# Optimization experiments

Hardware: AMD Instinct MI355X
Metric: run time of the kernel (lower is better)

Reference implementation:

```python
import jax, jax.numpy as jnp
import numpy as np

B, H, W, C, HEADS, SR = 4, 64, 64, 256, 8, 2
D = C // HEADS            # head dim = 32
SCALE = D ** -0.5
EPS = 1e-6


def _conv(x, w, stride, pad, groups):
    return jax.lax.conv_general_dilated(
        x, w, (stride, stride), [(pad, pad), (pad, pad)],
        feature_group_count=groups,
        dimension_numbers=('NCHW', 'OIHW', 'NCHW'))


def setup_inputs() -> dict:
    key = jax.random.key(0)
    ks = jax.random.split(key, 9)
    s = lambda fan: 1.0 / np.sqrt(fan)
    return {
        'x': jax.random.normal(ks[0], (B, H * W, C), jnp.float32),
        'dw_w': jax.random.normal(ks[1], (C, 1, 3, 3), jnp.float32) * s(9),
        'dw_b': jnp.zeros((C,), jnp.float32),
        'pw_w': jax.random.normal(ks[2], (C, C, 1, 1), jnp.float32) * s(C),
        'pw_b': jnp.zeros((C,), jnp.float32),
        'sr_w': jax.random.normal(ks[3], (C, 1, 3, 3), jnp.float32) * s(9),
        'ln_g': jnp.ones((C,), jnp.float32),
        'ln_b': jnp.zeros((C,), jnp.float32),
        'kv_w': jax.random.normal(ks[4], (2 * C, C), jnp.float32) * s(C),
        'kv_b': jnp.zeros((2 * C,), jnp.float32),
        'proj_w': jax.random.normal(ks[5], (C, C), jnp.float32) * s(C),
        'proj_b': jnp.zeros((C,), jnp.float32),
    }


def reference(x, dw_w, dw_b, pw_w, pw_b, sr_w, ln_g, ln_b, kv_w, kv_b, proj_w, proj_b):
    Bx, N, Cx = x.shape
    # Q path: depthwise-separable conv on the spatial layout
    xq = x.reshape(Bx, H, W, Cx).transpose(0, 3, 1, 2)          # (B,C,H,W)
    q = _conv(xq, dw_w, 1, 1, Cx) + dw_b[None, :, None, None]    # depthwise 3x3
    q = _conv(q, pw_w, 1, 0, 1) + pw_b[None, :, None, None]      # pointwise 1x1
    # 'b (h d) l w -> b h (l w) d'
    q = q.reshape(Bx, HEADS, D, H * W).transpose(0, 1, 3, 2)     # (B,h,N,d)

    # SR path for K/V: strided depthwise conv + LayerNorm
    x_ = _conv(xq, sr_w, SR, SR // 2, Cx)                        # (B,C,H/SR,W/SR)
    x_ = x_.reshape(Bx, Cx, -1).transpose(0, 2, 1)               # (B,M,C)
    mu = jnp.mean(x_, axis=-1, keepdims=True)
    var = jnp.mean(jnp.square(x_ - mu), axis=-1, keepdims=True)
    x_ = (x_ - mu) * jax.lax.rsqrt(var + EPS) * ln_g + ln_b

    kv = x_ @ kv_w.T + kv_b                                      # (B,M,2C)
    M = kv.shape[1]
    kv = kv.reshape(Bx, M, 2, HEADS, D).transpose(2, 0, 3, 1, 4) # (2,B,h,M,d)
    k, v = kv[0], kv[1]

    attn = jnp.einsum('bhnd,bhmd->bhnm', q, k) * SCALE           # (B,h,N,M)
    attn = jax.nn.softmax(attn, axis=-1)
    out = jnp.einsum('bhnm,bhmd->bhnd', attn, v)                 # (B,h,N,d)
    out = out.transpose(0, 2, 1, 3).reshape(Bx, N, Cx)           # (B,N,C)
    return out @ proj_w.T + proj_b
```

## Files before the change

kernel.cpp:

```cpp
#include <hip/hip_runtime.h>
#include <math.h>

#define BB 4
#define HH 64
#define WW 64
#define CC 256
#define NN 4096
#define MM 1024
#define LN_EPS 1e-6f
#define SLF (0.17677669529663687f * 1.4426950408889634f)

typedef __attribute__((ext_vector_type(8)))  short short8;
typedef __attribute__((ext_vector_type(16))) float f32x16;

__device__ __forceinline__ ushort f2bf(float f) {
  unsigned u = __builtin_bit_cast(unsigned, f);
  u += 0x7fffu + ((u >> 16) & 1u);
  return (ushort)(u >> 16);
}
__device__ __forceinline__ float bf2f(ushort h) {
  unsigned u = ((unsigned)h) << 16;
  return __builtin_bit_cast(float, u);
}
#if __has_builtin(__builtin_amdgcn_exp2f)
#define EXP2F(x) __builtin_amdgcn_exp2f(x)
#else
#define EXP2F(x) exp2f(x)
#endif

__global__ __launch_bounds__(256) void dwconv_kernel(
    const float* __restrict__ x, const float* __restrict__ w,
    const float* __restrict__ bias, ushort* __restrict__ out) {
  int c = threadIdx.x;
  int y = blockIdx.x >> 1, hf = blockIdx.x & 1;
  int b = blockIdx.y;
  float wr[9];
#pragma unroll
  for (int i = 0; i < 9; ++i) wr[i] = w[c * 9 + i];
  float bi = bias[c];
  const float* xb = x + (size_t)b * NN * CC + c;
  int x0 = hf * 32;
  bool okT = (y > 0), okB = (y < 63);
  float a0, a1, a2, b0, b1, b2;
  if (x0 == 0) {
    a0 = a1 = a2 = 0.f;
  } else {
    a0 = okT ? xb[(size_t)((y - 1) * 64 + x0 - 1) * CC] : 0.f;
    a1 = xb[(size_t)(y * 64 + x0 - 1) * CC];
    a2 = okB ? xb[(size_t)((y + 1) * 64 + x0 - 1) * CC] : 0.f;
  }
  b0 = okT ? xb[(size_t)((y - 1) * 64 + x0) * CC] : 0.f;
  b1 = xb[(size_t)(y * 64 + x0) * CC];
  b2 = okB ? xb[(size_t)((y + 1) * 64 + x0) * CC] : 0.f;
  ushort* ob = out + ((size_t)b * NN + y * 64) * CC + c;
#pragma unroll 8
  for (int xx = x0; xx < x0 + 32; ++xx) {
    float c0v, c1v, c2v;
    if (xx < 63) {
      c0v = okT ? xb[(size_t)((y - 1) * 64 + xx + 1) * CC] : 0.f;
      c1v = xb[(size_t)(y * 64 + xx + 1) * CC];
      c2v = okB ? xb[(size_t)((y + 1) * 64 + xx + 1) * CC] : 0.f;
    } else {
      c0v = c1v = c2v = 0.f;
    }
    float acc = bi;
    acc += a0 * wr[0] + b0 * wr[1] + c0v * wr[2];
    acc += a1 * wr[3] + b1 * wr[4] + c1v * wr[5];
    acc += a2 * wr[6] + b2 * wr[7] + c2v * wr[8];
    ob[(size_t)xx * CC] = f2bf(acc);
    a0 = b0; a1 = b1; a2 = b2;
    b0 = c0v; b1 = c1v; b2 = c2v;
  }
}

__global__ __launch_bounds__(256) void srln_kernel(
    const float* __restrict__ x, const float* __restrict__ w,
    const float* __restrict__ g, const float* __restrict__ beta,
    ushort* __restrict__ out) {
  int c = threadIdx.x;
  int m = blockIdx.x;
  int b = blockIdx.y;
  int my = m >> 5, mx = m & 31;
  const float* xb = x + (size_t)b * NN * CC + c;
  float acc = 0.f;
#pragma unroll
  for (int dy = 0; dy < 3; ++dy) {
    int iy = 2 * my + dy - 1;
    if (iy < 0 || iy >= HH) continue;
#pragma unroll
    for (int dx = 0; dx < 3; ++dx) {
      int ix = 2 * mx + dx - 1;
      if (ix < 0 || ix >= WW) continue;
      acc += xb[(size_t)(iy * WW + ix) * CC] * w[c * 9 + dy * 3 + dx];
    }
  }
  float v1 = acc, v2 = acc * acc;
#pragma unroll
  for (int s = 1; s < 64; s <<= 1) {
    v1 += __shfl_xor(v1, s);
    v2 += __shfl_xor(v2, s);
  }
  __shared__ float r1[4], r2[4];
  int lane = c & 63, wv = c >> 6;
  if (lane == 0) { r1[wv] = v1; r2[wv] = v2; }
  __syncthreads();
  float s1 = r1[0] + r1[1] + r1[2] + r1[3];
  float s2 = r2[0] + r2[1] + r2[2] + r2[3];
  float mu = s1 * (1.f / 256.f);
  float var = s2 * (1.f / 256.f) - mu * mu;
  float yv = (acc - mu) * rsqrtf(var + LN_EPS) * g[c] + beta[c];
  out[((size_t)b * MM + m) * CC + c] = f2bf(yv);
}

template <int MODE>
__global__ __launch_bounds__(256) void gemm_mfma(
    const ushort* __restrict__ A, const ushort* __restrict__ A2,
    const float* __restrict__ W, const float* __restrict__ bias,
    void* __restrict__ out0, void* __restrict__ out1) {
  extern __shared__ ushort smem[];
  constexpr int AS = 128 * 40, WS = 64 * 40;
  constexpr int OA = 0, OW = AS, OA2 = AS + WS, OW2 = 2 * AS + WS;
  constexpr int BUF = (MODE == 2) ? 2 * (AS + WS) : (AS + WS);
  ushort* bf0 = smem;
  ushort* bf1 = smem + BUF;

  int t = threadIdx.x;
  int lane = t & 63, w = t >> 6;
  int l31 = lane & 31, half = lane >> 5;
  int r0 = blockIdx.x * 128;
  int c0 = blockIdx.y * 64;
  const bool vmode = (MODE == 1) && (c0 >= 256);

  int rowA = t >> 2, kq = (t & 3) * 8;

  f32x16 acc[2];
#pragma unroll
  for (int ct = 0; ct < 2; ++ct)
#pragma unroll
    for (int i = 0; i < 16; ++i) acc[ct][i] = 0.f;

  short8 ra0, ra1, ra20, ra21;
  float4 rw0, rw1;

  auto prefetch = [&](int kc) {
    ra0 = *(const short8*)&A[(size_t)(r0 + rowA) * 256 + kc + kq];
    ra1 = *(const short8*)&A[(size_t)(r0 + rowA + 64) * 256 + kc + kq];
    const float* wp = &W[(size_t)(c0 + rowA) * 256 + kc + kq];
    rw0 = *(const float4*)wp;
    rw1 = *(const float4*)(wp + 4);
    if constexpr (MODE == 2) {
      ra20 = *(const short8*)&A2[(size_t)(r0 + rowA) * 256 + kc + kq];
      ra21 = *(const short8*)&A2[(size_t)(r0 + rowA + 64) * 256 + kc + kq];
    }
  };

  auto store = [&](ushort* buf) {
    *(short8*)&buf[OA + rowA * 40 + kq] = ra0;
    *(short8*)&buf[OA + (rowA + 64) * 40 + kq] = ra1;
    float vals[8] = {rw0.x, rw0.y, rw0.z, rw0.w, rw1.x, rw1.y, rw1.z, rw1.w};
    short8 hi;
#pragma unroll
    for (int j = 0; j < 8; ++j) hi[j] = (short)f2bf(vals[j]);
    *(short8*)&buf[OW + rowA * 40 + kq] = hi;
    if constexpr (MODE == 2) {
      *(short8*)&buf[OA2 + rowA * 40 + kq] = ra20;
      *(short8*)&buf[OA2 + (rowA + 64) * 40 + kq] = ra21;
      short8 lo;
#pragma unroll
      for (int j = 0; j < 8; ++j)
        lo[j] = (short)f2bf(vals[j] - bf2f((ushort)hi[j]));
      *(short8*)&buf[OW2 + rowA * 40 + kq] = lo;
    }
  };

  auto compute = [&](const ushort* buf) {
#pragma unroll
    for (int ks = 0; ks < 2; ++ks) {
      int ro = (w * 32 + l31) * 40 + ks * 16 + half * 8;
      short8 af = *(const short8*)&buf[OA + ro];
      short8 af2;
      if constexpr (MODE == 2) af2 = *(const short8*)&buf[OA2 + ro];
#pragma unroll
      for (int ct = 0; ct < 2; ++ct) {
        int co = (ct * 32 + l31) * 40 + ks * 16 + half * 8;
        short8 wf = *(const short8*)&buf[OW + co];
        if constexpr (MODE == 2) {
          short8 wf2 = *(const short8*)&buf[OW2 + co];
          acc[ct] = __builtin_amdgcn_mfma_f32_32x32x16_bf16(af, wf, acc[ct], 0, 0, 0);
          acc[ct] = __builtin_amdgcn_mfma_f32_32x32x16_bf16(af2, wf, acc[ct], 0, 0, 0);
          acc[ct] = __builtin_amdgcn_mfma_f32_32x32x16_bf16(af, wf2, acc[ct], 0, 0, 0);
        } else if (vmode) {
          acc[ct] = __builtin_amdgcn_mfma_f32_32x32x16_bf16(wf, af, acc[ct], 0, 0, 0);
        } else {
          acc[ct] = __builtin_amdgcn_mfma_f32_32x32x16_bf16(af, wf, acc[ct], 0, 0, 0);
        }
      }
    }
  };

  prefetch(0);
  store(bf0);
  __syncthreads();
  for (int i = 0; i < 8; ++i) {
    ushort* cur = (i & 1) ? bf1 : bf0;
    ushort* nxt = (i & 1) ? bf0 : bf1;
    if (i < 7) prefetch((i + 1) * 32);
    compute(cur);
    if (i < 7) store(nxt);
    __syncthreads();
  }

#pragma unroll
  for (int ct = 0; ct < 2; ++ct) {
#pragma unroll
    for (int i = 0; i < 16; ++i) {
      int rl = (i & 3) + 8 * (i >> 2) + 4 * half;
      if constexpr (MODE == 0) {
        int r = r0 + w * 32 + rl;
        int c = c0 + ct * 32 + l31;
        int b = r >> 12, n = r & 4095;
        int h = c >> 5, d = c & 31;
        float v = (acc[ct][i] + bias[c]) * SLF;
        ((ushort*)out0)[((size_t)(b * 8 + h) * NN + n) * 32 + d] = f2bf(v);
      } else if constexpr (MODE == 1) {
        if (!vmode) {
          int r = r0 + w * 32 + rl;
          int c = c0 + ct * 32 + l31;
          int b = r >> 10, m = r & 1023;
          int h = c >> 5, d = c & 31;
          ((ushort*)out0)[((size_t)(b * 8 + h) * MM + m) * 32 + d] =
              f2bf(acc[ct][i] + bias[c]);
        } else {
          int c = c0 + ct * 32 + rl;
          int r = r0 + w * 32 + l31;
          int b = r >> 10, m = r & 1023;
          int cv = c - 256;
          int h = cv >> 5, d = cv & 31;
          ((ushort*)out1)[((size_t)(b * 8 + h) * 32 + d) * MM + m] =
              f2bf(acc[ct][i] + bias[c]);
        }
      } else {
        int r = r0 + w * 32 + rl;
        int c = c0 + ct * 32 + l31;
        ((float*)out0)[(size_t)r * 256 + c] = acc[ct][i] + bias[c];
      }
    }
  }
}

__global__ __launch_bounds__(256, 4) void attn_mfma(
    const ushort* __restrict__ qB, const ushort* __restrict__ kB,
    const ushort* __restrict__ vT, ushort* __restrict__ aH,
    ushort* __restrict__ aL) {
  __shared__ ushort sK[2][64][40];
  __shared__ ushort sVt[2][32][72];
  __shared__ ushort sP[128][72];
  int t = threadIdx.x;
  int lane = t & 63, w = t >> 6;
  int l31 = lane & 31, half = lane >> 5;
  int bh = blockIdx.x;
  int b = bh >> 3, h = bh & 7;
  int q0 = blockIdx.y * 128;

  const ushort* qrow = qB + ((size_t)bh * NN + q0 + w * 32 + l31) * 32;
  short8 bq0 = *(const short8*)(qrow + half * 8);
  short8 bq1 = *(const short8*)(qrow + 16 + half * 8);

  const ushort* kbase = kB + (size_t)bh * MM * 32;
  const ushort* vbase = vT + (size_t)bh * 32 * MM;
  int krow = t >> 2, kq = (t & 3) * 8;
  int vd = t >> 3, vmo = (t & 7) * 8;

  short8 kreg = *(const short8*)&kbase[(size_t)krow * 32 + kq];
  short8 vreg = *(const short8*)&vbase[(size_t)vd * MM + vmo];
  *(short8*)&sK[0][krow][kq] = kreg;
  *(short8*)&sVt[0][vd][vmo] = vreg;

  float m_run = -3.0e38f, l_run = 0.f;
  f32x16 o;
#pragma unroll
  for (int i = 0; i < 16; ++i) o[i] = 0.f;
  __syncthreads();

  for (int mc = 0; mc < 16; ++mc) {
    int cur = mc & 1, nxt = cur ^ 1;
    if (mc < 15) {
      int m0n = (mc + 1) * 64;
      kreg = *(const short8*)&kbase[(size_t)(m0n + krow) * 32 + kq];
      vreg = *(const short8*)&vbase[(size_t)vd * MM + m0n + vmo];
    }
    f32x16 st[2];
#pragma unroll
    for (int tt = 0; tt < 2; ++tt) {
      short8 a0 = *(const short8*)&sK[cur][tt * 32 + l31][half * 8];
      short8 a1 = *(const short8*)&sK[cur][tt * 32 + l31][16 + half * 8];
      f32x16 z;
#pragma unroll
      for (int i = 0; i < 16; ++i) z[i] = 0.f;
      z = __builtin_amdgcn_mfma_f32_32x32x16_bf16(a0, bq0, z, 0, 0, 0);
      z = __builtin_amdgcn_mfma_f32_32x32x16_bf16(a1, bq1, z, 0, 0, 0);
      st[tt] = z;
    }

    float cm = st[0][0];
#pragma unroll
    for (int tt = 0; tt < 2; ++tt)
#pragma unroll
      for (int i = 0; i < 16; ++i) cm = fmaxf(cm, st[tt][i]);
    cm = fmaxf(cm, __shfl_xor(cm, 32));
    float nm = fmaxf(m_run, cm);
    float alpha = EXP2F(m_run - nm);
    float cs = 0.f;
#pragma unroll
    for (int tt = 0; tt < 2; ++tt) {
#pragma unroll
      for (int rg = 0; rg < 4; ++rg) {
        float p0 = EXP2F(st[tt][rg * 4 + 0] - nm);
        float p1 = EXP2F(st[tt][rg * 4 + 1] - nm);
        float p2 = EXP2F(st[tt][rg * 4 + 2] - nm);
        float p3 = EXP2F(st[tt][rg * 4 + 3] - nm);
        unsigned u0 = __builtin_bit_cast(unsigned, p0);
        unsigned u1 = __builtin_bit_cast(unsigned, p1);
        unsigned u2 = __builtin_bit_cast(unsigned, p2);
        unsigned u3 = __builtin_bit_cast(unsigned, p3);
        cs += __builtin_bit_cast(float, u0 & 0xffff0000u);
        cs += __builtin_bit_cast(float, u1 & 0xffff0000u);
        cs += __builtin_bit_cast(float, u2 & 0xffff0000u);
        cs += __builtin_bit_cast(float, u3 & 0xffff0000u);
        uint2 pk;
        pk.x = __builtin_amdgcn_perm(u1, u0, 0x07060302);
        pk.y = __builtin_amdgcn_perm(u3, u2, 0x07060302);
        *(uint2*)&sP[w * 32 + l31][tt * 32 + rg * 8 + half * 4] = pk;
      }
    }
    cs += __shfl_xor(cs, 32);
    l_run = l_run * alpha + cs;
    m_run = nm;
#pragma unroll
    for (int i = 0; i < 16; ++i) o[i] *= alpha;

#pragma unroll
    for (int kb = 0; kb < 4; ++kb) {
      short8 av = *(const short8*)&sVt[cur][l31][kb * 16 + half * 8];
      short8 bp = *(const short8*)&sP[w * 32 + l31][kb * 16 + half * 8];
      o = __builtin_amdgcn_mfma_f32_32x32x16_bf16(av, bp, o, 0, 0, 0);
    }

    if (mc < 15) {
      *(short8*)&sK[nxt][krow][kq] = kreg;
      *(short8*)&sVt[nxt][vd][vmo] = vreg;
    }
    __syncthreads();
  }

  float inv = 1.f / l_run;
  size_t rbase = ((size_t)b * NN + q0 + w * 32 + l31) * 256 + h * 32;
#pragma unroll
  for (int rg = 0; rg < 4; ++rg) {
#pragma unroll
    for (int j = 0; j < 4; ++j) {
      float v = o[rg * 4 + j] * inv;
      ushort hi = f2bf(v);
      ushort lo = f2bf(v - bf2f(hi));
      int d = rg * 8 + half * 4 + j;
      aH[rbase + d] = hi;
      aL[rbase + d] = lo;
    }
  }
}

extern "C" void kernel_launch(void* const* d_in, const int* in_sizes, int n_in,
                              void* d_out, int out_size, void* d_ws, size_t ws_size,
                              hipStream_t stream) {
  const float* x      = (const float*)d_in[0];
  const float* dw_w   = (const float*)d_in[1];
  const float* dw_b   = (const float*)d_in[2];
  const float* pw_w   = (const float*)d_in[3];
  const float* pw_b   = (const float*)d_in[4];
  const float* sr_w   = (const float*)d_in[5];
  const float* ln_g   = (const float*)d_in[6];
  const float* ln_b   = (const float*)d_in[7];
  const float* kv_w   = (const float*)d_in[8];
  const float* kv_b   = (const float*)d_in[9];
  const float* proj_w = (const float*)d_in[10];
  const float* proj_b = (const float*)d_in[11];
  float* out = (float*)d_out;

  char* ws = (char*)d_ws;
  ushort* q1b = (ushort*)(ws);
  ushort* xsr = (ushort*)(ws + (8u << 20));
  ushort* qB  = (ushort*)(ws + (16u << 20));
  ushort* kBp = (ushort*)(ws + (24u << 20));
  ushort* vTp = (ushort*)(ws + (26u << 20));
  ushort* aH  = (ushort*)(ws + (28u << 20));
  ushort* aL  = (ushort*)(ws + (36u << 20));

  const size_t smem_plain = 2 * (128 * 40 + 64 * 40) * sizeof(ushort);
  const size_t smem_proj  = 2 * smem_plain;

  dwconv_kernel<<<dim3(128, BB), 256, 0, stream>>>(x, dw_w, dw_b, q1b);
  srln_kernel<<<dim3(MM, BB), 256, 0, stream>>>(x, sr_w, ln_g, ln_b, xsr);
  gemm_mfma<0><<<dim3(128, 4), 256, smem_plain, stream>>>(
      q1b, nullptr, pw_w, pw_b, qB, nullptr);
  gemm_mfma<1><<<dim3(32, 8), 256, smem_plain, stream>>>(
      xsr, nullptr, kv_w, kv_b, kBp, vTp);
  attn_mfma<<<dim3(32, 32), 256, 0, stream>>>(qB, kBp, vTp, aH, aL);
  gemm_mfma<2><<<dim3(128, 4), 256, smem_proj, stream>>>(
      aH, aL, proj_w, proj_b, out, nullptr);
}
```

Measured before the change: 180.1 us.

## Merge pre-conv and QKV GEMM launches, shrink GEMM tiles to 64x64

The depthwise conv and the strided SR conv with LayerNorm now run in a single launch, with the block index choosing which branch runs. The pointwise Q GEMM and the KV GEMM are likewise merged into one launch. All GEMMs switch from 128x64 tiles to 64x64 tiles with a 2x2 wave grid, which gives more blocks and smaller static LDS. The projection GEMM drops double buffering and syncs twice per k-step. This removes two launches and fills the GPU better, at the cost of less reuse per tile and an unpipelined proj loop.

```diff
diff --git a/kernel.cpp b/kernel.cpp
--- a/kernel.cpp
+++ b/kernel.cpp
@@ -28,182 +28,156 @@
 #define EXP2F(x) exp2f(x)
 #endif
 
-__global__ __launch_bounds__(256) void dwconv_kernel(
-    const float* __restrict__ x, const float* __restrict__ w,
-    const float* __restrict__ bias, ushort* __restrict__ out) {
+__global__ __launch_bounds__(256) void pre_fused(
+    const float* __restrict__ x, const float* __restrict__ dw_w,
+    const float* __restrict__ dw_b, const float* __restrict__ sr_w,
+    const float* __restrict__ ln_g, const float* __restrict__ ln_b,
+    ushort* __restrict__ q1b, ushort* __restrict__ xsr) {
+  int bid = blockIdx.x;
   int c = threadIdx.x;
-  int y = blockIdx.x >> 1, hf = blockIdx.x & 1;
-  int b = blockIdx.y;
-  float wr[9];
-#pragma unroll
-  for (int i = 0; i < 9; ++i) wr[i] = w[c * 9 + i];
-  float bi = bias[c];
-  const float* xb = x + (size_t)b * NN * CC + c;
-  int x0 = hf * 32;
-  bool okT = (y > 0), okB = (y < 63);
-  float a0, a1, a2, b0, b1, b2;
-  if (x0 == 0) {
-    a0 = a1 = a2 = 0.f;
+  if (bid < 4096) {
+    int b = bid >> 10, m = bid & 1023;
+    int my = m >> 5, mx = m & 31;
+    const float* xb = x + (size_t)b * NN * CC + c;
+    float acc = 0.f;
+#pragma unroll
+    for (int dy = 0; dy < 3; ++dy) {
+      int iy = 2 * my + dy - 1;
+      if (iy < 0 || iy >= HH) continue;
+#pragma unroll
+      for (int dx = 0; dx < 3; ++dx) {
+        int ix = 2 * mx + dx - 1;
+        if (ix < 0 || ix >= WW) continue;
+        acc += xb[(size_t)(iy * WW + ix) * CC] * sr_w[c * 9 + dy * 3 + dx];
+      }
+    }
+    float v1 = acc, v2 = acc * acc;
+#pragma unroll
+    for (int s = 1; s < 64; s <<= 1) {
+      v1 += __shfl_xor(v1, s);
+      v2 += __shfl_xor(v2, s);
+    }
+    __shared__ float r1[4], r2[4];
+    int lane = c & 63, wv = c >> 6;
+    if (lane == 0) { r1[wv] = v1; r2[wv] = v2; }
+    __syncthreads();
+    float s1 = r1[0] + r1[1] + r1[2] + r1[3];
+    float s2 = r2[0] + r2[1] + r2[2] + r2[3];
+    float mu = s1 * (1.f / 256.f);
+    float var = s2 * (1.f / 256.f) - mu * mu;
+    float yv = (acc - mu) * rsqrtf(var + LN_EPS) * ln_g[c] + ln_b[c];
+    xsr[((size_t)b * MM + m) * CC + c] = f2bf(yv);
   } else {
-    a0 = okT ? xb[(size_t)((y - 1) * 64 + x0 - 1) * CC] : 0.f;
-    a1 = xb[(size_t)(y * 64 + x0 - 1) * CC];
-    a2 = okB ? xb[(size_t)((y + 1) * 64 + x0 - 1) * CC] : 0.f;
-  }
-  b0 = okT ? xb[(size_t)((y - 1) * 64 + x0) * CC] : 0.f;
-  b1 = xb[(size_t)(y * 64 + x0) * CC];
-  b2 = okB ? xb[(size_t)((y + 1) * 64 + x0) * CC] : 0.f;
-  ushort* ob = out + ((size_t)b * NN + y * 64) * CC + c;
+    int id = bid - 4096;
+    int b = id >> 7, yy = id & 127;
+    int y = yy >> 1, hf = yy & 1;
+    float wr[9];
+#pragma unroll
+    for (int i = 0; i < 9; ++i) wr[i] = dw_w[c * 9 + i];
+    float bi = dw_b[c];
+    const float* xb = x + (size_t)b * NN * CC + c;
+    int x0 = hf * 32;
+    bool okT = (y > 0), okB = (y < 63);
+    float a0, a1, a2, b0, b1, b2;
+    if (x0 == 0) {
+      a0 = a1 = a2 = 0.f;
+    } else {
+      a0 = okT ? xb[(size_t)((y - 1) * 64 + x0 - 1) * CC] : 0.f;
+      a1 = xb[(size_t)(y * 64 + x0 - 1) * CC];
+      a2 = okB ? xb[(size_t)((y + 1) * 64 + x0 - 1) * CC] : 0.f;
+    }
+    b0 = okT ? xb[(size_t)((y - 1) * 64 + x0) * CC] : 0.f;
+    b1 = xb[(size_t)(y * 64 + x0) * CC];
+    b2 = okB ? xb[(size_t)((y + 1) * 64 + x0) * CC] : 0.f;
+    ushort* ob = q1b + ((size_t)b * NN + y * 64) * CC + c;
 #pragma unroll 8
-  for (int xx = x0; xx < x0 + 32; ++xx) {
-    float c0v, c1v, c2v;
-    if (xx < 63) {
-      c0v = okT ? xb[(size_t)((y - 1) * 64 + xx + 1) * CC] : 0.f;
-      c1v = xb[(size_t)(y * 64 + xx + 1) * CC];
-      c2v = okB ? xb[(size_t)((y + 1) * 64 + xx + 1) * CC] : 0.f;
-    } else {
-      c0v = c1v = c2v = 0.f;
-    }
-    float acc = bi;
-    acc += a0 * wr[0] + b0 * wr[1] + c0v * wr[2];
-    acc += a1 * wr[3] + b1 * wr[4] + c1v * wr[5];
-    acc += a2 * wr[6] + b2 * wr[7] + c2v * wr[8];
-    ob[(size_t)xx * CC] = f2bf(acc);
-    a0 = b0; a1 = b1; a2 = b2;
-    b0 = c0v; b1 = c1v; b2 = c2v;
-  }
-}
-
-__global__ __launch_bounds__(256) void srln_kernel(
-    const float* __restrict__ x, const float* __restrict__ w,
-    const float* __restrict__ g, const float* __restrict__ beta,
-    ushort* __restrict__ out) {
-  int c = threadIdx.x;
-  int m = blockIdx.x;
-  int b = blockIdx.y;
-  int my = m >> 5, mx = m & 31;
-  const float* xb = x + (size_t)b * NN * CC + c;
-  float acc = 0.f;
-#pragma unroll
-  for (int dy = 0; dy < 3; ++dy) {
-    int iy = 2 * my + dy - 1;
-    if (iy < 0 || iy >= HH) continue;
-#pragma unroll
-    for (int dx = 0; dx < 3; ++dx) {
-      int ix = 2 * mx + dx - 1;
-      if (ix < 0 || ix >= WW) continue;
-      acc += xb[(size_t)(iy * WW + ix) * CC] * w[c * 9 + dy * 3 + dx];
-    }
-  }
-  float v1 = acc, v2 = acc * acc;
-#pragma unroll
-  for (int s = 1; s < 64; s <<= 1) {
-    v1 += __shfl_xor(v1, s);
-    v2 += __shfl_xor(v2, s);
-  }
-  __shared__ float r1[4], r2[4];
-  int lane = c & 63, wv = c >> 6;
-  if (lane == 0) { r1[wv] = v1; r2[wv] = v2; }
-  __syncthreads();
-  float s1 = r1[0] + r1[1] + r1[2] + r1[3];
-  float s2 = r2[0] + r2[1] + r2[2] + r2[3];
-  float mu = s1 * (1.f / 256.f);
-  float var = s2 * (1.f / 256.f) - mu * mu;
-  float yv = (acc - mu) * rsqrtf(var + LN_EPS) * g[c] + beta[c];
-  out[((size_t)b * MM + m) * CC + c] = f2bf(yv);
-}
-
-template <int MODE>
-__global__ __launch_bounds__(256) void gemm_mfma(
-    const ushort* __restrict__ A, const ushort* __restrict__ A2,
-    const float* __restrict__ W, const float* __restrict__ bias,
-    void* __restrict__ out0, void* __restrict__ out1) {
-  extern __shared__ ushort smem[];
-  constexpr int AS = 128 * 40, WS = 64 * 40;
-  constexpr int OA = 0, OW = AS, OA2 = AS + WS, OW2 = 2 * AS + WS;
-  constexpr int BUF = (MODE == 2) ? 2 * (AS + WS) : (AS + WS);
-  ushort* bf0 = smem;
-  ushort* bf1 = smem + BUF;
+    for (int xx = x0; xx < x0 + 32; ++xx) {
+      float c0v, c1v, c2v;
+      if (xx < 63) {
+        c0v = okT ? xb[(size_t)((y - 1) * 64 + xx + 1) * CC] : 0.f;
+        c1v = xb[(size_t)(y * 64 + xx + 1) * CC];
+        c2v = okB ? xb[(size_t)((y + 1) * 64 + xx + 1) * CC] : 0.f;
+      } else {
+        c0v = c1v = c2v = 0.f;
+      }
+      float acc = bi;
+      acc += a0 * wr[0] + b0 * wr[1] + c0v * wr[2];
+      acc += a1 * wr[3] + b1 * wr[4] + c1v * wr[5];
+      acc += a2 * wr[6] + b2 * wr[7] + c2v * wr[8];
+      ob[(size_t)xx * CC] = f2bf(acc);
+      a0 = b0; a1 = b1; a2 = b2;
+      b0 = c0v; b1 = c1v; b2 = c2v;
+    }
+  }
+}
+
+__global__ __launch_bounds__(256) void gemm_qkv(
+    const ushort* __restrict__ q1b, const ushort* __restrict__ xsr,
+    const float* __restrict__ pw_w, const float* __restrict__ pw_b,
+    const float* __restrict__ kv_w, const float* __restrict__ kv_b,
+    ushort* __restrict__ qB, ushort* __restrict__ kB,
+    ushort* __restrict__ vT) {
+  __shared__ ushort smem[2][128 * 40];
+  int bid = blockIdx.x;
+  bool is0 = bid < 1024;
+  const ushort* A;
+  const float* W;
+  const float* bias;
+  int r0, c0;
+  if (is0) {
+    A = q1b; W = pw_w; bias = pw_b;
+    r0 = (bid >> 2) * 64; c0 = (bid & 3) * 64;
+  } else {
+    int sid = bid - 1024;
+    A = xsr; W = kv_w; bias = kv_b;
+    r0 = (sid >> 3) * 64; c0 = (sid & 7) * 64;
+  }
+  const bool vmode = (!is0) && (c0 >= 256);
 
   int t = threadIdx.x;
   int lane = t & 63, w = t >> 6;
   int l31 = lane & 31, half = lane >> 5;
-  int r0 = blockIdx.x * 128;
-  int c0 = blockIdx.y * 64;
-  const bool vmode = (MODE == 1) && (c0 >= 256);
-
+  int wr = w >> 1, wc = w & 1;
   int rowA = t >> 2, kq = (t & 3) * 8;
 
-  f32x16 acc[2];
-#pragma unroll
-  for (int ct = 0; ct < 2; ++ct)
-#pragma unroll
-    for (int i = 0; i < 16; ++i) acc[ct][i] = 0.f;
-
-  short8 ra0, ra1, ra20, ra21;
+  f32x16 acc;
+#pragma unroll
+  for (int i = 0; i < 16; ++i) acc[i] = 0.f;
+
+  short8 ra;
   float4 rw0, rw1;
-
   auto prefetch = [&](int kc) {
-    ra0 = *(const short8*)&A[(size_t)(r0 + rowA) * 256 + kc + kq];
-    ra1 = *(const short8*)&A[(size_t)(r0 + rowA + 64) * 256 + kc + kq];
+    ra = *(const short8*)&A[(size_t)(r0 + rowA) * 256 + kc + kq];
     const float* wp = &W[(size_t)(c0 + rowA) * 256 + kc + kq];
     rw0 = *(const float4*)wp;
     rw1 = *(const float4*)(wp + 4);
-    if constexpr (MODE == 2) {
-      ra20 = *(const short8*)&A2[(size_t)(r0 + rowA) * 256 + kc + kq];
-      ra21 = *(const short8*)&A2[(size_t)(r0 + rowA + 64) * 256 + kc + kq];
-    }
   };
-
   auto store = [&](ushort* buf) {
-    *(short8*)&buf[OA + rowA * 40 + kq] = ra0;
-    *(short8*)&buf[OA + (rowA + 64) * 40 + kq] = ra1;
+    *(short8*)&buf[rowA * 40 + kq] = ra;
     float vals[8] = {rw0.x, rw0.y, rw0.z, rw0.w, rw1.x, rw1.y, rw1.z, rw1.w};
     short8 hi;
 #pragma unroll
     for (int j = 0; j < 8; ++j) hi[j] = (short)f2bf(vals[j]);
-    *(short8*)&buf[OW + rowA * 40 + kq] = hi;
-    if constexpr (MODE == 2) {
-      *(short8*)&buf[OA2 + rowA * 40 + kq] = ra20;
-      *(short8*)&buf[OA2 + (rowA + 64) * 40 + kq] = ra21;
-      short8 lo;
-#pragma unroll
-      for (int j = 0; j < 8; ++j)
-        lo[j] = (short)f2bf(vals[j] - bf2f((ushort)hi[j]));
-      *(short8*)&buf[OW2 + rowA * 40 + kq] = lo;
-    }
+    *(short8*)&buf[64 * 40 + rowA * 40 + kq] = hi;
   };
-
   auto compute = [&](const ushort* buf) {
 #pragma unroll
     for (int ks = 0; ks < 2; ++ks) {
-      int ro = (w * 32 + l31) * 40 + ks * 16 + half * 8;
-      short8 af = *(const short8*)&buf[OA + ro];
-      short8 af2;
-      if constexpr (MODE == 2) af2 = *(const short8*)&buf[OA2 + ro];
-#pragma unroll
-      for (int ct = 0; ct < 2; ++ct) {
-        int co = (ct * 32 + l31) * 40 + ks * 16 + half * 8;
-        short8 wf = *(const short8*)&buf[OW + co];
-        if constexpr (MODE == 2) {
-          short8 wf2 = *(const short8*)&buf[OW2 + co];
-          acc[ct] = __builtin_amdgcn_mfma_f32_32x32x16_bf16(af, wf, acc[ct], 0, 0, 0);
-          acc[ct] = __builtin_amdgcn_mfma_f32_32x32x16_bf16(af2, wf, acc[ct], 0, 0, 0);
-          acc[ct] = __builtin_amdgcn_mfma_f32_32x32x16_bf16(af, wf2, acc[ct], 0, 0, 0);
-        } else if (vmode) {
-          acc[ct] = __builtin_amdgcn_mfma_f32_32x32x16_bf16(wf, af, acc[ct], 0, 0, 0);
-        } else {
-          acc[ct] = __builtin_amdgcn_mfma_f32_32x32x16_bf16(af, wf, acc[ct], 0, 0, 0);
-        }
-      }
+      short8 af = *(const short8*)&buf[(wr * 32 + l31) * 40 + ks * 16 + half * 8];
+      short8 wf = *(const short8*)&buf[64 * 40 + (wc * 32 + l31) * 40 + ks * 16 + half * 8];
+      if (vmode)
+        acc = __builtin_amdgcn_mfma_f32_32x32x16_bf16(wf, af, acc, 0, 0, 0);
+      else
+        acc = __builtin_amdgcn_mfma_f32_32x32x16_bf16(af, wf, acc, 0, 0, 0);
     }
   };
 
   prefetch(0);
-  store(bf0);
+  store(smem[0]);
   __syncthreads();
   for (int i = 0; i < 8; ++i) {
-    ushort* cur = (i & 1) ? bf1 : bf0;
-    ushort* nxt = (i & 1) ? bf0 : bf1;
+    ushort* cur = smem[i & 1];
+    ushort* nxt = smem[(i & 1) ^ 1];
     if (i < 7) prefetch((i + 1) * 32);
     compute(cur);
     if (i < 7) store(nxt);
@@ -211,39 +185,28 @@
   }
 
 #pragma unroll
-  for (int ct = 0; ct < 2; ++ct) {
-#pragma unroll
-    for (int i = 0; i < 16; ++i) {
-      int rl = (i & 3) + 8 * (i >> 2) + 4 * half;
-      if constexpr (MODE == 0) {
-        int r = r0 + w * 32 + rl;
-        int c = c0 + ct * 32 + l31;
-        int b = r >> 12, n = r & 4095;
-        int h = c >> 5, d = c & 31;
-        float v = (acc[ct][i] + bias[c]) * SLF;
-        ((ushort*)out0)[((size_t)(b * 8 + h) * NN + n) * 32 + d] = f2bf(v);
-      } else if constexpr (MODE == 1) {
-        if (!vmode) {
-          int r = r0 + w * 32 + rl;
-          int c = c0 + ct * 32 + l31;
-          int b = r >> 10, m = r & 1023;
-          int h = c >> 5, d = c & 31;
-          ((ushort*)out0)[((size_t)(b * 8 + h) * MM + m) * 32 + d] =
-              f2bf(acc[ct][i] + bias[c]);
-        } else {
-          int c = c0 + ct * 32 + rl;
-          int r = r0 + w * 32 + l31;
-          int b = r >> 10, m = r & 1023;
-          int cv = c - 256;
-          int h = cv >> 5, d = cv & 31;
-          ((ushort*)out1)[((size_t)(b * 8 + h) * 32 + d) * MM + m] =
-              f2bf(acc[ct][i] + bias[c]);
-        }
-      } else {
-        int r = r0 + w * 32 + rl;
-        int c = c0 + ct * 32 + l31;
-        ((float*)out0)[(size_t)r * 256 + c] = acc[ct][i] + bias[c];
-      }
+  for (int i = 0; i < 16; ++i) {
+    int rl = (i & 3) + 8 * (i >> 2) + 4 * half;
+    if (is0) {
+      int r = r0 + wr * 32 + rl;
+      int c = c0 + wc * 32 + l31;
+      int b = r >> 12, n = r & 4095;
+      int h = c >> 5, d = c & 31;
+      qB[((size_t)(b * 8 + h) * NN + n) * 32 + d] =
+          f2bf((acc[i] + bias[c]) * SLF);
+    } else if (!vmode) {
+      int r = r0 + wr * 32 + rl;
+      int c = c0 + wc * 32 + l31;
+      int b = r >> 10, m = r & 1023;
+      int h = c >> 5, d = c & 31;
+      kB[((size_t)(b * 8 + h) * MM + m) * 32 + d] = f2bf(acc[i] + bias[c]);
+    } else {
+      int c = c0 + wc * 32 + rl;
+      int r = r0 + wr * 32 + l31;
+      int b = r >> 10, m = r & 1023;
+      int cv = c - 256;
+      int h = cv >> 5, d = cv & 31;
+      vT[((size_t)(b * 8 + h) * 32 + d) * MM + m] = f2bf(acc[i] + bias[c]);
     }
   }
 }
@@ -369,6 +332,81 @@
   }
 }
 
+__global__ __launch_bounds__(256) void gemm_proj(
+    const ushort* __restrict__ A, const ushort* __restrict__ A2,
+    const float* __restrict__ W, const float* __restrict__ bias,
+    float* __restrict__ out) {
+  __shared__ ushort smem[4 * 64 * 40];
+  constexpr int OA = 0, OA2 = 64 * 40, OW = 2 * 64 * 40, OW2 = 3 * 64 * 40;
+  int bid = blockIdx.x;
+  int r0 = (bid >> 2) * 64, c0 = (bid & 3) * 64;
+
+  int t = threadIdx.x;
+  int lane = t & 63, w = t >> 6;
+  int l31 = lane & 31, half = lane >> 5;
+  int wr = w >> 1, wc = w & 1;
+  int rowA = t >> 2, kq = (t & 3) * 8;
+
+  f32x16 acc;
+#pragma unroll
+  for (int i = 0; i < 16; ++i) acc[i] = 0.f;
+
+  short8 ra, ra2;
+  float4 rw0, rw1;
+  auto prefetch = [&](int kc) {
+    ra = *(const short8*)&A[(size_t)(r0 + rowA) * 256 + kc + kq];
+    ra2 = *(const short8*)&A2[(size_t)(r0 + rowA) * 256 + kc + kq];
+    const float* wp = &W[(size_t)(c0 + rowA) * 256 + kc + kq];
+    rw0 = *(const float4*)wp;
+    rw1 = *(const float4*)(wp + 4);
+  };
+  auto store = [&]() {
+    *(short8*)&smem[OA + rowA * 40 + kq] = ra;
+    *(short8*)&smem[OA2 + rowA * 40 + kq] = ra2;
+    float vals[8] = {rw0.x, rw0.y, rw0.z, rw0.w, rw1.x, rw1.y, rw1.z, rw1.w};
+    short8 hi, lo;
+#pragma unroll
+    for (int j = 0; j < 8; ++j) {
+      hi[j] = (short)f2bf(vals[j]);
+      lo[j] = (short)f2bf(vals[j] - bf2f((ushort)hi[j]));
+    }
+    *(short8*)&smem[OW + rowA * 40 + kq] = hi;
+    *(short8*)&smem[OW2 + rowA * 40 + kq] = lo;
+  };
+
+  prefetch(0);
+  store();
+  __syncthreads();
+  for (int i = 0; i < 8; ++i) {
+    if (i < 7) prefetch((i + 1) * 32);
+#pragma unroll
+    for (int ks = 0; ks < 2; ++ks) {
+      int ro = (wr * 32 + l31) * 40 + ks * 16 + half * 8;
+      int co = (wc * 32 + l31) * 40 + ks * 16 + half * 8;
+      short8 af = *(const short8*)&smem[OA + ro];
+      short8 af2 = *(const short8*)&smem[OA2 + ro];
+      short8 wf = *(const short8*)&smem[OW + co];
+      short8 wf2 = *(const short8*)&smem[OW2 + co];
+      acc = __builtin_amdgcn_mfma_f32_32x32x16_bf16(af, wf, acc, 0, 0, 0);
+      acc = __builtin_amdgcn_mfma_f32_32x32x16_bf16(af2, wf, acc, 0, 0, 0);
+      acc = __builtin_amdgcn_mfma_f32_32x32x16_bf16(af, wf2, acc, 0, 0, 0);
+    }
+    __syncthreads();
+    if (i < 7) {
+      store();
+      __syncthreads();
+    }
+  }
+
+#pragma unroll
+  for (int i = 0; i < 16; ++i) {
+    int rl = (i & 3) + 8 * (i >> 2) + 4 * half;
+    int r = r0 + wr * 32 + rl;
+    int c = c0 + wc * 32 + l31;
+    out[(size_t)r * 256 + c] = acc[i] + bias[c];
+  }
+}
+
 extern "C" void kernel_launch(void* const* d_in, const int* in_sizes, int n_in,
                               void* d_out, int out_size, void* d_ws, size_t ws_size,
                               hipStream_t stream) {
@@ -395,16 +433,10 @@
   ushort* aH  = (ushort*)(ws + (28u << 20));
   ushort* aL  = (ushort*)(ws + (36u << 20));
 
-  const size_t smem_plain = 2 * (128 * 40 + 64 * 40) * sizeof(ushort);
-  const size_t smem_proj  = 2 * smem_plain;
-
-  dwconv_kernel<<<dim3(128, BB), 256, 0, stream>>>(x, dw_w, dw_b, q1b);
-  srln_kernel<<<dim3(MM, BB), 256, 0, stream>>>(x, sr_w, ln_g, ln_b, xsr);
-  gemm_mfma<0><<<dim3(128, 4), 256, smem_plain, stream>>>(
-      q1b, nullptr, pw_w, pw_b, qB, nullptr);
-  gemm_mfma<1><<<dim3(32, 8), 256, smem_plain, stream>>>(
-      xsr, nullptr, kv_w, kv_b, kBp, vTp);
+  pre_fused<<<dim3(4608), 256, 0, stream>>>(x, dw_w, dw_b, sr_w, ln_g, ln_b,
+                                            q1b, xsr);
+  gemm_qkv<<<dim3(1536), 256, 0, stream>>>(q1b, xsr, pw_w, pw_b, kv_w, kv_b,
+                                           qB, kBp, vTp);
   attn_mfma<<<dim3(32, 32), 256, 0, stream>>>(qB, kBp, vTp, aH, aL);
-  gemm_mfma<2><<<dim3(128, 4), 256, smem_proj, stream>>>(
-      aH, aL, proj_w, proj_b, out, nullptr);
-}
+  gemm_proj<<<dim3(1024), 256, 0, stream>>>(aH, aL, proj_w, proj_b, out);
+}
```

Result: faster. 171.7 us (-4.6%).
